# Optimization experiments

Hardware: AMD Instinct MI355X
Metric: run time of the kernel (lower is better)

## Reference

```python
import jax, jax.numpy as jnp
import numpy as np

NUM_LATENTS = 32768
NUM_EMBEDDINGS = 1024
EMBEDDING_SIZE = 64


def setup_inputs() -> dict:
    key = jax.random.key(0)
    kx, ke = jax.random.split(key)
    x = jax.random.normal(kx, (NUM_LATENTS * EMBEDDING_SIZE,), dtype=jnp.float32)
    # uniform init in [-limit, limit], limit = sqrt(3/embedding_size) as in the torch module
    limit = float(np.sqrt(3.0 / EMBEDDING_SIZE))
    embeddings = jax.random.uniform(
        ke, (NUM_EMBEDDINGS, EMBEDDING_SIZE), dtype=jnp.float32,
        minval=-limit, maxval=limit)
    return {"x": x, "embeddings": embeddings}


def reference(x, embeddings):
    K, E = embeddings.shape
    x_ = x.reshape(-1, E)  # [L, E]
    # squared distances ||x - e||^2 expanded: faithful to sum((x-e)**2, -1), fused as one GEMM
    d = (
        jnp.sum(x_ * x_, axis=-1, keepdims=True)
        - 2.0 * jnp.einsum('le,ke->lk', x_, embeddings)
        + jnp.sum(embeddings * embeddings, axis=-1)
    )  # [L, K]
    indices = jnp.argmin(d, axis=-1)          # [L]
    quantized = embeddings[indices].reshape(-1)  # [L*E]
    # straight-through estimator: x + (q - stop_grad(x))
    z_hat = x + quantized - jax.lax.stop_gradient(x)
    # outputs mirror the torch dict: z_continuous, z_quantized, z_hat, z_indices
    return x, quantized, z_hat, indices
```

## Files before the change

### kernel.cpp

```cpp
#include <hip/hip_runtime.h>

#define L_TOTAL   32768
#define E_DIM     64
#define K_TOTAL   1024
#define NT_TOTAL  64
#define OUT_STRIDE 2097152

typedef _Float16 half_t;
typedef _Float16 half8  __attribute__((ext_vector_type(8)));
typedef float    floatx4 __attribute__((ext_vector_type(4)));

#define WS_EHS 0u
#define WS_ELS 131072u
#define WS_ENS 262144u

__global__ __launch_bounds__(128)
void vq_swizzle_kernel(const float* __restrict__ emb,
                       half_t* __restrict__ ehs, half_t* __restrict__ els,
                       float* __restrict__ ens) {
    __shared__ float s_p[128];
    __shared__ float s_n[16];
    const int nt   = blockIdx.x;
    const int t    = threadIdx.x;
    const int kt   = t >> 6;
    const int lane = t & 63;
    const int q    = lane >> 4;
    const int ln   = lane & 15;

    const float* src = emb + (size_t)(nt * 16 + ln) * E_DIM + kt * 32 + q * 8;
    float4 v0 = *(const float4*)src;
    float4 v1 = *(const float4*)(src + 4);
    float f[8] = {v0.x, v0.y, v0.z, v0.w, v1.x, v1.y, v1.z, v1.w};

    half8 h, l;
    float s = 0.f;
    #pragma unroll
    for (int j = 0; j < 8; ++j) {
        half_t hh = (half_t)f[j];
        half_t ll = (half_t)(f[j] - (float)hh);
        h[j] = hh;
        l[j] = ll;
        s = fmaf(f[j], f[j], s);
    }
    const size_t fo = ((size_t)(nt * 2 + kt) * 64 + lane) * 8;
    *(half8*)(ehs + fo) = h;
    *(half8*)(els + fo) = l;

    s_p[t] = s;
    __syncthreads();
    if (t < 16) {
        float n = 0.f;
        #pragma unroll
        for (int u = 0; u < 8; ++u)
            n += s_p[(u >> 2) * 64 + (u & 3) * 16 + t];
        s_n[t] = n;
    }
    __syncthreads();
    if (t < 64) ens[nt * 64 + t] = s_n[t & 15];
}

__global__ __launch_bounds__(256, 2)
void vq_fused_kernel(const float* __restrict__ x,
                     const float* __restrict__ emb,
                     const half_t* __restrict__ ehs, const half_t* __restrict__ els,
                     const float* __restrict__ ens,
                     float* __restrict__ out) {
    __shared__ float s_best[4][64];
    __shared__ int   s_bidx[4][64];
    __shared__ int   s_fin[64];

    const int tid   = threadIdx.x;
    const int ks    = tid >> 6;
    const int lane  = tid & 63;
    const int q     = lane >> 4;
    const int ln    = lane & 15;
    const int mbase = blockIdx.x * 64;
    const int off   = (blockIdx.x >> 3) & 15;

    half8 A[4][2][2];
    float nrm[4];
    #pragma unroll
    for (int rt = 0; rt < 4; ++rt) {
        const float* xr = x + (size_t)(mbase + rt * 16 + ln) * E_DIM + q * 8;
        float s = 0.f;
        #pragma unroll
        for (int kt = 0; kt < 2; ++kt) {
            float4 v0 = *(const float4*)(xr + kt * 32);
            float4 v1 = *(const float4*)(xr + kt * 32 + 4);
            float f[8] = {v0.x, v0.y, v0.z, v0.w, v1.x, v1.y, v1.z, v1.w};
            #pragma unroll
            for (int j = 0; j < 8; ++j) {
                half_t hh = (half_t)f[j];
                half_t ll = (half_t)(f[j] - (float)hh);
                A[rt][kt][0][j] = hh;
                A[rt][kt][1][j] = ll;
                s = fmaf(f[j], f[j], s);
            }
        }
        s += __shfl_xor(s, 16, 64);
        s += __shfl_xor(s, 32, 64);
        nrm[rt] = s;
    }
    floatx4 xq[4];
    #pragma unroll
    for (int rt = 0; rt < 4; ++rt)
        #pragma unroll
        for (int r = 0; r < 4; ++r)
            xq[rt][r] = __shfl(nrm[rt], q * 4 + r, 64);

    float best[4][4];
    int   bidx[4][4];
    #pragma unroll
    for (int rt = 0; rt < 4; ++rt)
        #pragma unroll
        for (int r = 0; r < 4; ++r) { best[rt][r] = 3.402823466e+38f; bidx[rt][r] = 0x7fffffff; }

    const int kq = ks * 16;

    #pragma unroll 2
    for (int j = 0; j < 16; ++j) {
        const int nt = kq + ((j + off) & 15);
        const half8 bh0 = *(const half8*)(ehs + ((size_t)(nt * 2 + 0) * 64 + lane) * 8);
        const half8 bh1 = *(const half8*)(ehs + ((size_t)(nt * 2 + 1) * 64 + lane) * 8);
        const half8 bl0 = *(const half8*)(els + ((size_t)(nt * 2 + 0) * 64 + lane) * 8);
        const half8 bl1 = *(const half8*)(els + ((size_t)(nt * 2 + 1) * 64 + lane) * 8);
        const float env = ens[nt * 64 + lane];
        const int   kg  = nt * 16 + ln;

        #pragma unroll
        for (int rt = 0; rt < 4; ++rt) {
            floatx4 Ca = {0.f, 0.f, 0.f, 0.f};
            floatx4 Cb = {0.f, 0.f, 0.f, 0.f};
            Ca = __builtin_amdgcn_mfma_f32_16x16x32_f16(A[rt][0][0], bh0, Ca, 0, 0, 0);
            Ca = __builtin_amdgcn_mfma_f32_16x16x32_f16(A[rt][1][0], bh1, Ca, 0, 0, 0);
            Cb = __builtin_amdgcn_mfma_f32_16x16x32_f16(A[rt][0][1], bh0, Cb, 0, 0, 0);
            Cb = __builtin_amdgcn_mfma_f32_16x16x32_f16(A[rt][1][1], bh1, Cb, 0, 0, 0);
            Cb = __builtin_amdgcn_mfma_f32_16x16x32_f16(A[rt][0][0], bl0, Cb, 0, 0, 0);
            Cb = __builtin_amdgcn_mfma_f32_16x16x32_f16(A[rt][1][0], bl1, Cb, 0, 0, 0);
            #pragma unroll
            for (int r = 0; r < 4; ++r) {
                float dot = Ca[r] + Cb[r];
                float d = __fadd_rn(__fsub_rn(xq[rt][r], __fmul_rn(2.0f, dot)), env);
                if (d < best[rt][r] || (d == best[rt][r] && kg < bidx[rt][r])) {
                    best[rt][r] = d; bidx[rt][r] = kg;
                }
            }
        }
    }

    #pragma unroll
    for (int o = 1; o < 16; o <<= 1) {
        #pragma unroll
        for (int rt = 0; rt < 4; ++rt)
            #pragma unroll
            for (int r = 0; r < 4; ++r) {
                float ob = __shfl_xor(best[rt][r], o, 64);
                int   oi = __shfl_xor(bidx[rt][r], o, 64);
                if (ob < best[rt][r] || (ob == best[rt][r] && oi < bidx[rt][r])) {
                    best[rt][r] = ob; bidx[rt][r] = oi;
                }
            }
    }
    if (ln == 0) {
        #pragma unroll
        for (int rt = 0; rt < 4; ++rt)
            #pragma unroll
            for (int r = 0; r < 4; ++r) {
                s_best[ks][rt * 16 + q * 4 + r] = best[rt][r];
                s_bidx[ks][rt * 16 + q * 4 + r] = bidx[rt][r];
            }
    }
    __syncthreads();

    if (tid < 64) {
        float b = 3.402823466e+38f;
        int   i = 0x7fffffff;
        #pragma unroll
        for (int s = 0; s < 4; ++s) {
            float pb = s_best[s][tid];
            int   pi = s_bidx[s][tid];
            if (pb < b || (pb == b && pi < i)) { b = pb; i = pi; }
        }
        s_fin[tid] = i;
        out[3 * (size_t)OUT_STRIDE + mbase + tid] = (float)i;
    }
    __syncthreads();

    if (ks == 0) {
        #pragma unroll
        for (int rt = 0; rt < 4; ++rt) {
            float* dst = out + (size_t)(mbase + rt * 16 + ln) * E_DIM + q * 8;
            #pragma unroll
            for (int kt = 0; kt < 2; ++kt) {
                float4 u, v;
                u.x = (float)A[rt][kt][0][0] + (float)A[rt][kt][1][0];
                u.y = (float)A[rt][kt][0][1] + (float)A[rt][kt][1][1];
                u.z = (float)A[rt][kt][0][2] + (float)A[rt][kt][1][2];
                u.w = (float)A[rt][kt][0][3] + (float)A[rt][kt][1][3];
                v.x = (float)A[rt][kt][0][4] + (float)A[rt][kt][1][4];
                v.y = (float)A[rt][kt][0][5] + (float)A[rt][kt][1][5];
                v.z = (float)A[rt][kt][0][6] + (float)A[rt][kt][1][6];
                v.w = (float)A[rt][kt][0][7] + (float)A[rt][kt][1][7];
                *(float4*)(dst + kt * 32)     = u;
                *(float4*)(dst + kt * 32 + 4) = v;
            }
        }
    } else if (ks == 1) {
        #pragma unroll
        for (int rt = 0; rt < 4; ++rt) {
            const int idx = s_fin[rt * 16 + ln];
            const float* ep = emb + (size_t)idx * E_DIM + q * 8;
            float* dst = out + (size_t)OUT_STRIDE + (size_t)(mbase + rt * 16 + ln) * E_DIM + q * 8;
            #pragma unroll
            for (int kt = 0; kt < 2; ++kt) {
                *(float4*)(dst + kt * 32)     = *(const float4*)(ep + kt * 32);
                *(float4*)(dst + kt * 32 + 4) = *(const float4*)(ep + kt * 32 + 4);
            }
        }
    } else if (ks == 2) {
        #pragma unroll
        for (int rt = 0; rt < 4; ++rt) {
            const int idx = s_fin[rt * 16 + ln];
            const float* ep = emb + (size_t)idx * E_DIM + q * 8;
            float* dst = out + 2 * (size_t)OUT_STRIDE + (size_t)(mbase + rt * 16 + ln) * E_DIM + q * 8;
            #pragma unroll
            for (int kt = 0; kt < 2; ++kt) {
                float4 qv0 = *(const float4*)(ep + kt * 32);
                float4 qv1 = *(const float4*)(ep + kt * 32 + 4);
                float qq[8] = {qv0.x, qv0.y, qv0.z, qv0.w, qv1.x, qv1.y, qv1.z, qv1.w};
                float z[8];
                #pragma unroll
                for (int j = 0; j < 8; ++j) {
                    float xt = (float)A[rt][kt][0][j] + (float)A[rt][kt][1][j];
                    z[j] = __fsub_rn(__fadd_rn(xt, qq[j]), xt);
                }
                *(float4*)(dst + kt * 32)     = make_float4(z[0], z[1], z[2], z[3]);
                *(float4*)(dst + kt * 32 + 4) = make_float4(z[4], z[5], z[6], z[7]);
            }
        }
    }
}

extern "C" void kernel_launch(void* const* d_in, const int* in_sizes, int n_in,
                              void* d_out, int out_size, void* d_ws, size_t ws_size,
                              hipStream_t stream) {
    const float* x   = (const float*)d_in[0];
    const float* emb = (const float*)d_in[1];
    float* out = (float*)d_out;

    char* ws = (char*)d_ws;
    half_t* ehs = (half_t*)(ws + WS_EHS);
    half_t* els = (half_t*)(ws + WS_ELS);
    float*  ens = (float*)(ws + WS_ENS);

    hipLaunchKernelGGL(vq_swizzle_kernel, dim3(NT_TOTAL), dim3(128), 0, stream,
                       emb, ehs, els, ens);
    hipLaunchKernelGGL(vq_fused_kernel, dim3(L_TOTAL / 64), dim3(256), 0, stream,
                       x, emb, ehs, els, ens, out);
}
```

Baseline: 97.08 us.

## Stage x tile in LDS and coalesce epilogue writes across all warps

The 64-row x tile is now loaded cooperatively into padded shared memory with fully coalesced float4 loads, and the A fragments are built from LDS instead of strided global reads. The epilogue no longer splits the three outputs across three of the four wavefronts with per-lane strided stores. All 256 threads now write contiguous float4 chunks of x, quantized and z_hat from LDS and the embedding table. This uses all warps and makes stores coalesced, at the cost of 17KB of extra LDS per block, which may reduce occupancy.

```diff
diff --git a/kernel.cpp b/kernel.cpp
--- a/kernel.cpp
+++ b/kernel.cpp
@@ -5,6 +5,7 @@
 #define K_TOTAL   1024
 #define NT_TOTAL  64
 #define OUT_STRIDE 2097152
+#define XPAD      68
 
 typedef _Float16 half_t;
 typedef _Float16 half8  __attribute__((ext_vector_type(8)));
@@ -65,6 +66,7 @@
                      const half_t* __restrict__ ehs, const half_t* __restrict__ els,
                      const float* __restrict__ ens,
                      float* __restrict__ out) {
+    __shared__ float s_x[64 * XPAD];
     __shared__ float s_best[4][64];
     __shared__ int   s_bidx[4][64];
     __shared__ int   s_fin[64];
@@ -77,11 +79,23 @@
     const int mbase = blockIdx.x * 64;
     const int off   = (blockIdx.x >> 3) & 15;
 
+    {
+        const float4* xg = (const float4*)(x + (size_t)mbase * E_DIM);
+        #pragma unroll
+        for (int i = 0; i < 4; ++i) {
+            const int f   = i * 256 + tid;
+            const int row = f >> 4;
+            const int col = (f & 15) * 4;
+            *(float4*)(&s_x[row * XPAD + col]) = xg[f];
+        }
+    }
+    __syncthreads();
+
     half8 A[4][2][2];
     float nrm[4];
     #pragma unroll
     for (int rt = 0; rt < 4; ++rt) {
-        const float* xr = x + (size_t)(mbase + rt * 16 + ln) * E_DIM + q * 8;
+        const float* xr = &s_x[(rt * 16 + ln) * XPAD + q * 8];
         float s = 0.f;
         #pragma unroll
         for (int kt = 0; kt < 2; ++kt) {
@@ -186,57 +200,27 @@
     }
     __syncthreads();
 
-    if (ks == 0) {
-        #pragma unroll
-        for (int rt = 0; rt < 4; ++rt) {
-            float* dst = out + (size_t)(mbase + rt * 16 + ln) * E_DIM + q * 8;
-            #pragma unroll
-            for (int kt = 0; kt < 2; ++kt) {
-                float4 u, v;
-                u.x = (float)A[rt][kt][0][0] + (float)A[rt][kt][1][0];
-                u.y = (float)A[rt][kt][0][1] + (float)A[rt][kt][1][1];
-                u.z = (float)A[rt][kt][0][2] + (float)A[rt][kt][1][2];
-                u.w = (float)A[rt][kt][0][3] + (float)A[rt][kt][1][3];
-                v.x = (float)A[rt][kt][0][4] + (float)A[rt][kt][1][4];
-                v.y = (float)A[rt][kt][0][5] + (float)A[rt][kt][1][5];
-                v.z = (float)A[rt][kt][0][6] + (float)A[rt][kt][1][6];
-                v.w = (float)A[rt][kt][0][7] + (float)A[rt][kt][1][7];
-                *(float4*)(dst + kt * 32)     = u;
-                *(float4*)(dst + kt * 32 + 4) = v;
-            }
-        }
-    } else if (ks == 1) {
-        #pragma unroll
-        for (int rt = 0; rt < 4; ++rt) {
-            const int idx = s_fin[rt * 16 + ln];
-            const float* ep = emb + (size_t)idx * E_DIM + q * 8;
-            float* dst = out + (size_t)OUT_STRIDE + (size_t)(mbase + rt * 16 + ln) * E_DIM + q * 8;
-            #pragma unroll
-            for (int kt = 0; kt < 2; ++kt) {
-                *(float4*)(dst + kt * 32)     = *(const float4*)(ep + kt * 32);
-                *(float4*)(dst + kt * 32 + 4) = *(const float4*)(ep + kt * 32 + 4);
-            }
-        }
-    } else if (ks == 2) {
-        #pragma unroll
-        for (int rt = 0; rt < 4; ++rt) {
-            const int idx = s_fin[rt * 16 + ln];
-            const float* ep = emb + (size_t)idx * E_DIM + q * 8;
-            float* dst = out + 2 * (size_t)OUT_STRIDE + (size_t)(mbase + rt * 16 + ln) * E_DIM + q * 8;
-            #pragma unroll
-            for (int kt = 0; kt < 2; ++kt) {
-                float4 qv0 = *(const float4*)(ep + kt * 32);
-                float4 qv1 = *(const float4*)(ep + kt * 32 + 4);
-                float qq[8] = {qv0.x, qv0.y, qv0.z, qv0.w, qv1.x, qv1.y, qv1.z, qv1.w};
-                float z[8];
-                #pragma unroll
-                for (int j = 0; j < 8; ++j) {
-                    float xt = (float)A[rt][kt][0][j] + (float)A[rt][kt][1][j];
-                    z[j] = __fsub_rn(__fadd_rn(xt, qq[j]), xt);
-                }
-                *(float4*)(dst + kt * 32)     = make_float4(z[0], z[1], z[2], z[3]);
-                *(float4*)(dst + kt * 32 + 4) = make_float4(z[4], z[5], z[6], z[7]);
-            }
+    {
+        const size_t base = (size_t)mbase * (E_DIM / 4);
+        float4* o0 = (float4*)out + base;
+        float4* o1 = (float4*)(out + OUT_STRIDE) + base;
+        float4* o2 = (float4*)(out + 2 * (size_t)OUT_STRIDE) + base;
+        #pragma unroll
+        for (int i = 0; i < 4; ++i) {
+            const int f   = i * 256 + tid;
+            const int row = f >> 4;
+            const int col = (f & 15) * 4;
+            const float4 xv = *(const float4*)(&s_x[row * XPAD + col]);
+            const int idx = s_fin[row];
+            const float4 qv = *(const float4*)(emb + (size_t)idx * E_DIM + col);
+            float4 z;
+            z.x = __fsub_rn(__fadd_rn(xv.x, qv.x), xv.x);
+            z.y = __fsub_rn(__fadd_rn(xv.y, qv.y), xv.y);
+            z.z = __fsub_rn(__fadd_rn(xv.z, qv.z), xv.z);
+            z.w = __fsub_rn(__fadd_rn(xv.w, qv.w), xv.w);
+            o0[f] = xv;
+            o1[f] = qv;
+            o2[f] = z;
         }
     }
 }
```

Measured after the change: 94.63 us. -2.5%, faster.
